# Performance work log

Hardware: AMD Instinct MI355X
Metric: run time of the kernel (lower is better)

The kernel has to match this reference:

```python
import jax, jax.numpy as jnp
import numpy as np

UP = 2
NUM_POINT = 9
GROUPS = 4


def pixel_shuffle(t, r):
    # [B, C*r*r, H, W] -> [B, C, H*r, W*r], torch layout: in[b, c*r*r + i*r + j, h, w] -> out[b, c, h*r+i, w*r+j]
    B, C, H, W = t.shape
    Co = C // (r * r)
    t = t.reshape(B, Co, r, r, H, W)
    t = t.transpose(0, 1, 4, 2, 5, 3)
    return t.reshape(B, Co, H * r, W * r)


def _bilinear_sample(feat, py, px):
    # feat: [E, H, W]; py, px: [P, Hup, Wup] in low-res pixel coords (zero padding outside)
    H, W = feat.shape[1], feat.shape[2]
    y0f = jnp.floor(py)
    x0f = jnp.floor(px)
    ty = py - y0f
    tx = px - x0f
    y0 = y0f.astype(jnp.int32)
    x0 = x0f.astype(jnp.int32)
    out = jnp.zeros(feat.shape[:1] + py.shape, dtype=feat.dtype)
    corners = ((0, 0, (1 - ty) * (1 - tx)), (0, 1, (1 - ty) * tx),
               (1, 0, ty * (1 - tx)), (1, 1, ty * tx))
    for dy, dx, w in corners:
        yi = y0 + dy
        xi = x0 + dx
        valid = ((yi >= 0) & (yi < H) & (xi >= 0) & (xi < W)).astype(feat.dtype)
        yc = jnp.clip(yi, 0, H - 1)
        xc = jnp.clip(xi, 0, W - 1)
        out = out + feat[:, yc, xc] * (w * valid)[None]
    return out  # [E, P, Hup, Wup]

# vmap over batch and group dims
_sample_bg = jax.vmap(jax.vmap(_bilinear_sample))


def setup_inputs() -> dict:
    key = jax.random.key(0)
    ks = jax.random.split(key, 8)
    B, Cy, Cx = 2, 256, 256
    H, W = 64, 64
    Hup, Wup = H * UP, W * UP
    GE = GROUPS * 32              # q/k channels = groups * embedding_dim
    OFF = GROUPS * NUM_POINT * 2 * UP * UP  # 288
    return {
        "y": jax.random.normal(ks[0], (B, Cy, Hup, Wup), jnp.float32),
        "x": jax.random.normal(ks[1], (B, Cx, H, W), jnp.float32),
        "Wq": jax.random.normal(ks[2], (GE, Cy), jnp.float32) * 0.02,
        "bq": jnp.zeros((GE,), jnp.float32),
        "Wk": jax.random.normal(ks[3], (GE, Cx), jnp.float32) * 0.02,
        "bk": jnp.zeros((GE,), jnp.float32),
        "Woff": jax.random.normal(ks[4], (OFF, Cx), jnp.float32) * 0.02,
        "boff": jnp.zeros((OFF,), jnp.float32),
    }


def reference(y, x, Wq, bq, Wk, bk, Woff, boff):
    G, P, up = GROUPS, NUM_POINT, UP
    B, C, H, W = x.shape
    # 1x1 convs as einsum
    q = jnp.einsum('oi,bihw->bohw', Wq, y) + bq[None, :, None, None]
    k = jnp.einsum('oi,bihw->bohw', Wk, x) + bk[None, :, None, None]
    off = jnp.einsum('oi,bihw->bohw', Woff, x) + boff[None, :, None, None]
    off = pixel_shuffle(off, up)  # [B, G*P*2, Hup, Wup]
    Hup, Wup = off.shape[2], off.shape[3]
    off = off.reshape(B, G, P, 2, Hup, Wup)
    # sampling positions in low-res coordinates: align-centers base + learned offset
    base_y = (jnp.arange(Hup, dtype=jnp.float32) + 0.5) / up - 0.5
    base_x = (jnp.arange(Wup, dtype=jnp.float32) + 0.5) / up - 0.5
    py = off[:, :, :, 0] + base_y[None, None, None, :, None]  # [B,G,P,Hup,Wup]
    px = off[:, :, :, 1] + base_x[None, None, None, None, :]
    E = Wq.shape[0] // G
    qg = q.reshape(B, G, E, Hup, Wup)
    kg = k.reshape(B, G, E, H, W)
    # deform_qk: gather k at offset points, dot with q over embedding dim
    ks = _sample_bg(kg, py, px)                    # [B,G,E,P,Hup,Wup]
    attn = jnp.einsum('bgehw,bgephw->bgphw', qg, ks)
    attn = jax.nn.softmax(attn, axis=2)            # softmax over points
    # deform_av: gather x at the same points, weighted sum by attn
    Cg = C // G
    xg = x.reshape(B, G, Cg, H, W)
    xs = _sample_bg(xg, py, px)                    # [B,G,Cg,P,Hup,Wup]
    out = jnp.einsum('bgphw,bgcphw->bgchw', attn, xs)
    return out.reshape(B, C, Hup, Wup)
```

## Files before the change

### kernel.cpp

```cpp
#include <hip/hip_runtime.h>

#define B_N   2
#define H_LR  64
#define W_LR  64
#define HUP   128
#define WUP   128
#define GRP   4
#define NPT   9
#define EMB   32
#define CGRP  64
#define KIN   256
#define GE    128
#define NOFF  288

typedef __attribute__((ext_vector_type(8))) short short8v;
typedef _Float16 half8v __attribute__((ext_vector_type(8)));
typedef __attribute__((ext_vector_type(4))) float f32x4;

__device__ __forceinline__ ushort f2bf(float f) {
    unsigned u = __float_as_uint(f);
    u += 0x7FFFu + ((u >> 16) & 1u);
    return (ushort)(u >> 16);
}
__device__ __forceinline__ float bf2f(ushort h) {
    return __uint_as_float(((unsigned)h) << 16);
}
__device__ __forceinline__ ushort f2h(float f) {
    _Float16 h = (_Float16)f;
    return __builtin_bit_cast(ushort, h);
}
__device__ __forceinline__ float h2f(ushort u) {
    _Float16 h = __builtin_bit_cast(_Float16, u);
    return (float)h;
}

__global__ __launch_bounds__(256) void convert_w_kernel(
    const float* __restrict__ Wq, const float* __restrict__ Wk,
    const float* __restrict__ Woff, ushort* __restrict__ wqbf,
    ushort* __restrict__ wkobf)
{
    int r = blockIdx.x, k = threadIdx.x;
    if (r < 128) {
        wqbf[r * 256 + k] = f2bf(Wq[r * 256 + k]);
    } else {
        int r2 = r - 128;
        float v = 0.f;
        if (r2 < 128) v = Wk[r2 * 256 + k];
        else if (r2 < 416) v = Woff[(r2 - 128) * 256 + k];
        wkobf[r2 * 256 + k] = f2bf(v);
    }
}

__global__ __launch_bounds__(256, 4) void mfma_gemm(
    const float* __restrict__ y, const float* __restrict__ x,
    const ushort* __restrict__ WQ, const ushort* __restrict__ WKO,
    const float* __restrict__ bq, const float* __restrict__ bk,
    const float* __restrict__ boff,
    ushort* __restrict__ qbf, ushort* __restrict__ kbf,
    float* __restrict__ offw)
{
    __shared__ __align__(16) ushort sY[64][68];
    __shared__ __align__(16) ushort sB[128][72];

    int bid = blockIdx.x;
    const float* SRC; const ushort* WBF; const float* ba; const float* bb;
    ushort* OBF; float* OFP;
    int M, m0, n0, b;
    if (bid < 512) {
        int mt = bid & 255; b = bid >> 8;
        SRC = y; WBF = WQ; ba = bq; bb = nullptr; OBF = qbf; OFP = nullptr;
        M = 16384; m0 = mt * 64; n0 = 0;
    } else {
        int r = bid - 512;
        int mt = r & 63, nt2 = (r >> 6) & 3; b = r >> 8;
        SRC = x; WBF = WKO; ba = bk; bb = boff; OBF = kbf; OFP = offw;
        M = 4096; m0 = mt * 64; n0 = nt2 * 128;
    }

    int tid = threadIdx.x;
    int lane = tid & 63;
    int wv = tid >> 6, wm = wv >> 1, wn = wv & 1;
    int il = lane & 15, g4 = lane >> 4;
    int st_m4 = tid & 15, st_c = tid >> 4;
    int st_c8 = tid & 7,  st_n = tid >> 3;

    f32x4 acc[2][4];
#pragma unroll
    for (int i = 0; i < 2; ++i)
#pragma unroll
        for (int j = 0; j < 4; ++j) { f32x4 z = {0.f,0.f,0.f,0.f}; acc[i][j] = z; }

    const float* src_b = SRC + (size_t)b * KIN * M;

    float4 ra[4]; short8v rb[4];
#pragma unroll
    for (int i = 0; i < 4; ++i)
        ra[i] = *(const float4*)&src_b[(size_t)(st_c + i * 16) * M + m0 + st_m4 * 4];
#pragma unroll
    for (int i = 0; i < 4; ++i)
        rb[i] = *(const short8v*)&WBF[(size_t)(n0 + st_n + i * 32) * KIN + st_c8 * 8];

    for (int ks = 0; ks < 4; ++ks) {
#pragma unroll
        for (int i = 0; i < 4; ++i) {
            ushort4 h;
            h.x = f2bf(ra[i].x); h.y = f2bf(ra[i].y);
            h.z = f2bf(ra[i].z); h.w = f2bf(ra[i].w);
            *(ushort4*)&sY[st_c + i * 16][st_m4 * 4] = h;
            *(short8v*)&sB[st_n + i * 32][st_c8 * 8] = rb[i];
        }
        __syncthreads();
        if (ks < 3) {
            int k0 = (ks + 1) * 64;
#pragma unroll
            for (int i = 0; i < 4; ++i)
                ra[i] = *(const float4*)&src_b[(size_t)(k0 + st_c + i * 16) * M + m0 + st_m4 * 4];
#pragma unroll
            for (int i = 0; i < 4; ++i)
                rb[i] = *(const short8v*)&WBF[(size_t)(n0 + st_n + i * 32) * KIN + k0 + st_c8 * 8];
        }
#pragma unroll
        for (int kc = 0; kc < 2; ++kc) {
            int kb = kc * 32 + g4 * 8;
            short8v af[2], bfr[4];
#pragma unroll
            for (int mf = 0; mf < 2; ++mf) {
                int m = wm * 32 + mf * 16 + il;
                short8v t;
#pragma unroll
                for (int j = 0; j < 8; ++j) t[j] = (short)sY[kb + j][m];
                af[mf] = t;
            }
#pragma unroll
            for (int nf = 0; nf < 4; ++nf)
                bfr[nf] = *(const short8v*)&sB[wn * 64 + nf * 16 + il][kb];
#pragma unroll
            for (int mf = 0; mf < 2; ++mf)
#pragma unroll
                for (int nf = 0; nf < 4; ++nf)
                    acc[mf][nf] = __builtin_amdgcn_mfma_f32_16x16x32_bf16(
                        af[mf], bfr[nf], acc[mf][nf], 0, 0, 0);
        }
        __syncthreads();
    }

#pragma unroll
    for (int mf = 0; mf < 2; ++mf) {
#pragma unroll
        for (int r = 0; r < 4; ++r) {
            int m = m0 + wm * 32 + mf * 16 + g4 * 4 + r;
            size_t row = (size_t)b * M + m;
#pragma unroll
            for (int nf = 0; nf < 4; ++nf) {
                int n = n0 + wn * 64 + nf * 16 + il;
                float v = acc[mf][nf][r];
                if (n < GE) {
                    OBF[row * 128 + n] = f2bf(v + ba[n]);
                } else {
                    int no = n - GE;
                    if (no < NOFF) OFP[row * 288 + no] = v + bb[no];
                }
            }
        }
    }
}

#define RROWS 6
#define RCOLS 11
#define RPX   66

__global__ __launch_bounds__(256, 4) void deform_kernel(
    const ushort* __restrict__ qbf,
    const ushort* __restrict__ kbf,
    const float* __restrict__ offw,
    const float* __restrict__ x,
    float* __restrict__ out)
{
    __shared__ __align__(16) ushort sXt[64][96];
    __shared__ __align__(16) ushort sK[66][40];
    __shared__ __align__(16) ushort sQ[64][40];
    __shared__ __align__(16) ushort sSW[64][72];
    __shared__ uint   sGt[576];
    __shared__ int    sGz[576];
    __shared__ float  sAttn[576];
    __shared__ int    sFB[129];

    int bx = blockIdx.x;
    int tw = bx & 7, th = (bx >> 3) & 31, g = (bx >> 8) & 3, b = bx >> 10;
    int tid = threadIdx.x;
    int wv_ = tid >> 6, lane = tid & 63;
    int row = lane & 15, kb8 = lane >> 4;

    const int ry0 = th * 2 - 2, rx0 = tw * 8 - 1;
    float* sOff = (float*)&sSW[0][0];

    if (tid == 0) sFB[0] = 0;
    for (int i = tid; i < 960; i += 256) {
        int r = i / 15, j = i - (i / 15) * 15;
        *(uint*)&sXt[r][66 + j * 2] = 0;
    }
    for (int s = tid; s < 384; s += 256) {
        int gy = s % 6, ch = s / 6;
        int gyg = min(max(ry0 + gy, 0), 63);
        const float* xr = x + ((size_t)b * 256 + g * CGRP + ch) * 4096 + gyg * 64;
        ushort* dst = &sXt[ch][gy * RCOLS];
        if (tw >= 1 && tw <= 6) {
            int a0 = rx0 - 3;
            float v[16];
#pragma unroll
            for (int t4 = 0; t4 < 4; ++t4) {
                float4 f = *(const float4*)&xr[a0 + t4 * 4];
                v[t4*4+0] = f.x; v[t4*4+1] = f.y; v[t4*4+2] = f.z; v[t4*4+3] = f.w;
            }
#pragma unroll
            for (int qx = 0; qx < RCOLS; ++qx) dst[qx] = f2h(v[qx + 3]);
        } else {
#pragma unroll
            for (int qx = 0; qx < RCOLS; ++qx) {
                int gxg = min(max(rx0 + qx, 0), 63);
                dst[qx] = f2h(xr[gxg]);
            }
        }
    }
    for (int i = tid; i < 264; i += 256) {
        int rp = i >> 2, c4 = i & 3;
        int qy = rp / RCOLS, qx = rp - qy * RCOLS;
        int gy = min(max(ry0 + qy, 0), 63), gx = min(max(rx0 + qx, 0), 63);
        *(short8v*)&sK[rp][c4 * 8] =
            *(const short8v*)&kbf[((size_t)b * 4096 + gy * 64 + gx) * 128 +
                                  g * EMB + c4 * 8];
    }
    {
        int px = tid >> 2, c4 = tid & 3;
        int hup = th * 4 + (px >> 4), wup = tw * 16 + (px & 15);
        *(short8v*)&sQ[px][c4 * 8] =
            *(const short8v*)&qbf[((size_t)b * 16384 + hup * 128 + wup) * 128 +
                                  g * EMB + c4 * 8];
    }
    for (int i = tid; i < 288; i += 256) {
        int lr = i / 18, f4 = i - (i / 18) * 18;
        int yy = th * 2 + (lr >> 3), xx = tw * 8 + (lr & 7);
        *(float4*)&sOff[lr * 72 + f4 * 4] =
            *(const float4*)&offw[((size_t)b * 4096 + yy * 64 + xx) * 288 +
                                  g * 72 + f4 * 4];
    }
    __syncthreads();

    f32x4 sreg[5];
    {
        short8v a = *(const short8v*)&sQ[wv_ * 16 + row][kb8 * 8];
#pragma unroll
        for (int nt = 0; nt < 5; ++nt) {
            int rr = nt * 16 + row; if (rr > 65) rr = 65;
            short8v bf = *(const short8v*)&sK[rr][kb8 * 8];
            f32x4 z = {0.f, 0.f, 0.f, 0.f};
            sreg[nt] = __builtin_amdgcn_mfma_f32_16x16x32_bf16(a, bf, z, 0, 0, 0);
        }
    }
    for (int item = tid; item < 576; item += 256) {
        int px = item / 9, pt = item - (item / 9) * 9;
        int lx = px & 15, ly = px >> 4;
        int hup = th * 4 + ly, wup = tw * 16 + lx;
        int lr = (ly >> 1) * 8 + (lx >> 1);
        int ij = ((hup & 1) << 1) | (wup & 1);
        float offy = sOff[lr * 72 + pt * 8 + ij];
        float offx = sOff[lr * 72 + pt * 8 + 4 + ij];
        float py  = offy + hup * 0.5f - 0.25f;
        float pxx = offx + wup * 0.5f - 0.25f;
        float y0f = floorf(py), x0f = floorf(pxx);
        float ty = py - y0f, tx = pxx - x0f;
        int y0 = (int)y0f, x0 = (int)x0f;
        int mk = 0;
        if ((unsigned)y0 < 64u && (unsigned)x0 < 64u)         mk |= 1;
        if ((unsigned)y0 < 64u && (unsigned)(x0+1) < 64u)     mk |= 2;
        if ((unsigned)(y0+1) < 64u && (unsigned)x0 < 64u)     mk |= 4;
        if ((unsigned)(y0+1) < 64u && (unsigned)(x0+1) < 64u) mk |= 8;
        int iy = y0 - ry0, ix = x0 - rx0;
        bool inreg = ((unsigned)iy <= (unsigned)(RROWS - 2)) &&
                     ((unsigned)ix <= (unsigned)(RCOLS - 2));
        int fl, zp;
        if (!mk)        { fl = 16; zp = 0; }
        else if (inreg) { fl = mk | 16; zp = iy * RCOLS + ix; }
        else            { fl = mk; zp = (y0 + 1) * 66 + (x0 + 1); }
        sGt[item] = (uint)f2h(ty) | ((uint)f2h(tx) << 16);
        sGz[item] = (zp << 5) | fl;
    }
    __syncthreads();

#pragma unroll
    for (int nt = 0; nt < 5; ++nt) {
        int rp = nt * 16 + row;
        if (rp < RPX) {
#pragma unroll
            for (int r = 0; r < 4; ++r)
                sSW[wv_ * 16 + kb8 * 4 + r][rp] = f2h(sreg[nt][r]);
        }
    }
    __syncthreads();

    for (int item = tid; item < 576; item += 256) {
        int px = item / 9;
        uint gt = sGt[item];
        float ty = h2f((ushort)gt), tx = h2f((ushort)(gt >> 16));
        int z = sGz[item];
        int fl = z & 31;
        float a;
        if (fl & 16) {
            int zi = z >> 5;
            float w00 = (1.f - ty) * (1.f - tx), w01 = (1.f - ty) * tx;
            float w10 = ty * (1.f - tx), w11 = ty * tx;
            a  = (fl & 1) ? w00 * h2f(sSW[px][zi])             : 0.f;
            a += (fl & 2) ? w01 * h2f(sSW[px][zi + 1])         : 0.f;
            a += (fl & 4) ? w10 * h2f(sSW[px][zi + RCOLS])     : 0.f;
            a += (fl & 8) ? w11 * h2f(sSW[px][zi + RCOLS + 1]) : 0.f;
        } else {
            int t = z >> 5;
            int y0 = t / 66 - 1, x0 = t - (t / 66) * 66 - 1;
            a = 0.f;
#pragma unroll
            for (int c = 0; c < 4; ++c) if ((fl >> c) & 1) {
                int dy = c >> 1, dx = c & 1;
                float wgt = (dy ? ty : 1.f - ty) * (dx ? tx : 1.f - tx);
                const ushort* kr = &kbf[((size_t)b * 4096 + (y0 + dy) * 64 + x0 + dx) * 128 +
                                        g * EMB];
                float dot = 0.f;
                for (int e = 0; e < EMB; ++e) dot += bf2f(sQ[px][e]) * bf2f(kr[e]);
                a += wgt * dot;
            }
            int old = atomicAdd(&sFB[0], 1);
            if (old < 128) sFB[1 + old] = item;
        }
        sAttn[item] = a;
    }
    __syncthreads();

    if (tid < 64) {
        float aa[NPT];
        float mx = -1e30f;
#pragma unroll
        for (int p = 0; p < NPT; ++p) { aa[p] = sAttn[tid * 9 + p]; mx = fmaxf(mx, aa[p]); }
        float s = 0.f;
#pragma unroll
        for (int p = 0; p < NPT; ++p) { aa[p] = __expf(aa[p] - mx); s += aa[p]; }
        float inv = 1.f / s;
#pragma unroll
        for (int p = 0; p < NPT; ++p) sAttn[tid * 9 + p] = aa[p] * inv;
    } else {
        float4* p = (float4*)&sSW[0][0];
        float4 z4 = make_float4(0.f, 0.f, 0.f, 0.f);
        for (int i = tid - 64; i < 576; i += 192) p[i] = z4;
    }
    __syncthreads();

    if (tid < 64) {
        int px = tid;
#pragma unroll
        for (int pt = 0; pt < NPT; ++pt) {
            int item = px * 9 + pt;
            int z = sGz[item];
            int fl = z & 31;
            if (!(fl & 16)) continue;
            uint gt = sGt[item];
            float ty = h2f((ushort)gt), tx = h2f((ushort)(gt >> 16));
            float a = sAttn[item];
            int zi = z >> 5;
            ushort* c = &sSW[px][zi];
            if (fl & 1) c[0]         = f2h(h2f(c[0])         + (1.f-ty)*(1.f-tx)*a);
            if (fl & 2) c[1]         = f2h(h2f(c[1])         + (1.f-ty)*tx*a);
            if (fl & 4) c[RCOLS]     = f2h(h2f(c[RCOLS])     + ty*(1.f-tx)*a);
            if (fl & 8) c[RCOLS + 1] = f2h(h2f(c[RCOLS + 1]) + ty*tx*a);
        }
    }
    __syncthreads();

    {
        half8v bfm[3][4];
#pragma unroll
        for (int kt = 0; kt < 3; ++kt)
#pragma unroll
            for (int nt = 0; nt < 4; ++nt)
                bfm[kt][nt] = *(const half8v*)&sXt[nt * 16 + row][kt * 32 + kb8 * 8];

        int px = wv_ * 16 + row;
        half8v af0 = *(const half8v*)&sSW[px][kb8 * 8];
        half8v af1 = *(const half8v*)&sSW[px][32 + kb8 * 8];
        half8v af2 = {0,0,0,0,0,0,0,0};
        if (kb8 == 0) af2 = *(const half8v*)&sSW[px][64];

        f32x4 acc[4];
#pragma unroll
        for (int nt = 0; nt < 4; ++nt) { f32x4 z = {0.f,0.f,0.f,0.f}; acc[nt] = z; }
#pragma unroll
        for (int nt = 0; nt < 4; ++nt) {
            acc[nt] = __builtin_amdgcn_mfma_f32_16x16x32_f16(af0, bfm[0][nt], acc[nt], 0, 0, 0);
            acc[nt] = __builtin_amdgcn_mfma_f32_16x16x32_f16(af1, bfm[1][nt], acc[nt], 0, 0, 0);
            acc[nt] = __builtin_amdgcn_mfma_f32_16x16x32_f16(af2, bfm[2][nt], acc[nt], 0, 0, 0);
        }
        int hup = th * 4 + wv_;
#pragma unroll
        for (int nt = 0; nt < 4; ++nt) {
            int ch = nt * 16 + row;
            float* ob = out + ((size_t)b * 256 + g * CGRP + ch) * 16384 +
                        hup * 128 + tw * 16 + kb8 * 4;
#pragma unroll
            for (int r = 0; r < 4; ++r) ob[r] = acc[nt][r];
        }
    }
    __syncthreads();

    int nfb = min(sFB[0], 128);
    for (int i = 0; i < nfb; ++i) {
        if (tid < 64) {
            int item = sFB[1 + i];
            int px = item / 9;
            uint gt = sGt[item];
            float ty = h2f((ushort)gt), tx = h2f((ushort)(gt >> 16));
            int z = sGz[item];
            float a = sAttn[item];
            int fl = z & 15;
            int t = z >> 5;
            int y0 = t / 66 - 1, x0 = t - (t / 66) * 66 - 1;
            const float* xg = x + ((size_t)b * 256 + g * CGRP + tid) * 4096;
            float v = 0.f;
            if (fl & 1) v += (1.f-ty)*(1.f-tx)*a * xg[y0*64 + x0];
            if (fl & 2) v += (1.f-ty)*tx*a       * xg[y0*64 + x0 + 1];
            if (fl & 4) v += ty*(1.f-tx)*a       * xg[(y0+1)*64 + x0];
            if (fl & 8) v += ty*tx*a             * xg[(y0+1)*64 + x0 + 1];
            int hup = th * 4 + (px >> 4), wup = tw * 16 + (px & 15);
            float* op = out + ((size_t)b * 256 + g * CGRP + tid) * 16384 +
                        hup * 128 + wup;
            *op += v;
        }
    }
}

extern "C" void kernel_launch(void* const* d_in, const int* in_sizes, int n_in,
                              void* d_out, int out_size, void* d_ws, size_t ws_size,
                              hipStream_t stream)
{
    const float* y    = (const float*)d_in[0];
    const float* x    = (const float*)d_in[1];
    const float* Wq   = (const float*)d_in[2];
    const float* bq   = (const float*)d_in[3];
    const float* Wk   = (const float*)d_in[4];
    const float* bk   = (const float*)d_in[5];
    const float* Woff = (const float*)d_in[6];
    const float* boff = (const float*)d_in[7];
    float* out = (float*)d_out;

    ushort* wqbf  = (ushort*)d_ws;
    ushort* wkobf = wqbf + 128 * 256;
    ushort* qbf   = wkobf + 512 * 256;
    ushort* kbf   = qbf + (size_t)B_N * 16384 * 128;
    float*  offw  = (float*)(kbf + (size_t)B_N * 4096 * 128);

    convert_w_kernel<<<dim3(640), dim3(256), 0, stream>>>(Wq, Wk, Woff, wqbf, wkobf);

    mfma_gemm<<<dim3(1024), dim3(256), 0, stream>>>(
        y, x, wqbf, wkobf, bq, bk, boff, qbf, kbf, offw);

    deform_kernel<<<dim3(2048), dim3(256), 0, stream>>>(qbf, kbf, offw, x, out);
}
```

Before: 64.86 us.

## Fuse weight bf16 conversion into GEMM and trim deform MFMA tail

Drops the separate weight-conversion kernel. The GEMM now reads fp32 weights directly and converts them to bf16 while staging, which saves one launch and a workspace round trip but repeats the conversion in every block. In the deform kernel, the sXt row is narrowed and its zero-padding pass removed, and the x tile is written with packed 32-bit stores. The third MFMA over a mostly-zero K chunk is replaced by a two-term scalar FMA tail on the leftover columns.

```diff
diff --git a/kernel.cpp b/kernel.cpp
--- a/kernel.cpp
+++ b/kernel.cpp
@@ -34,26 +34,10 @@
     return (float)h;
 }
 
-__global__ __launch_bounds__(256) void convert_w_kernel(
-    const float* __restrict__ Wq, const float* __restrict__ Wk,
-    const float* __restrict__ Woff, ushort* __restrict__ wqbf,
-    ushort* __restrict__ wkobf)
-{
-    int r = blockIdx.x, k = threadIdx.x;
-    if (r < 128) {
-        wqbf[r * 256 + k] = f2bf(Wq[r * 256 + k]);
-    } else {
-        int r2 = r - 128;
-        float v = 0.f;
-        if (r2 < 128) v = Wk[r2 * 256 + k];
-        else if (r2 < 416) v = Woff[(r2 - 128) * 256 + k];
-        wkobf[r2 * 256 + k] = f2bf(v);
-    }
-}
-
 __global__ __launch_bounds__(256, 4) void mfma_gemm(
     const float* __restrict__ y, const float* __restrict__ x,
-    const ushort* __restrict__ WQ, const ushort* __restrict__ WKO,
+    const float* __restrict__ Wq, const float* __restrict__ Wk,
+    const float* __restrict__ Woff,
     const float* __restrict__ bq, const float* __restrict__ bk,
     const float* __restrict__ boff,
     ushort* __restrict__ qbf, ushort* __restrict__ kbf,
@@ -63,17 +47,18 @@
     __shared__ __align__(16) ushort sB[128][72];
 
     int bid = blockIdx.x;
-    const float* SRC; const ushort* WBF; const float* ba; const float* bb;
+    const float* SRC; const float* ba; const float* bb;
     ushort* OBF; float* OFP;
     int M, m0, n0, b;
-    if (bid < 512) {
+    bool isQ = (bid < 512);
+    if (isQ) {
         int mt = bid & 255; b = bid >> 8;
-        SRC = y; WBF = WQ; ba = bq; bb = nullptr; OBF = qbf; OFP = nullptr;
+        SRC = y; ba = bq; bb = nullptr; OBF = qbf; OFP = nullptr;
         M = 16384; m0 = mt * 64; n0 = 0;
     } else {
         int r = bid - 512;
         int mt = r & 63, nt2 = (r >> 6) & 3; b = r >> 8;
-        SRC = x; WBF = WKO; ba = bk; bb = boff; OBF = kbf; OFP = offw;
+        SRC = x; ba = bk; bb = boff; OBF = kbf; OFP = offw;
         M = 4096; m0 = mt * 64; n0 = nt2 * 128;
     }
 
@@ -84,6 +69,16 @@
     int st_m4 = tid & 15, st_c = tid >> 4;
     int st_c8 = tid & 7,  st_n = tid >> 3;
 
+    const float* wrowp[4];
+#pragma unroll
+    for (int i = 0; i < 4; ++i) {
+        int n = n0 + st_n + i * 32;
+        if (isQ)            wrowp[i] = Wq  + (size_t)n * KIN;
+        else if (n < GE)    wrowp[i] = Wk  + (size_t)n * KIN;
+        else if (n < GE + NOFF) wrowp[i] = Woff + (size_t)(n - GE) * KIN;
+        else                wrowp[i] = nullptr;
+    }
+
     f32x4 acc[2][4];
 #pragma unroll
     for (int i = 0; i < 2; ++i)
@@ -97,8 +92,16 @@
     for (int i = 0; i < 4; ++i)
         ra[i] = *(const float4*)&src_b[(size_t)(st_c + i * 16) * M + m0 + st_m4 * 4];
 #pragma unroll
-    for (int i = 0; i < 4; ++i)
-        rb[i] = *(const short8v*)&WBF[(size_t)(n0 + st_n + i * 32) * KIN + st_c8 * 8];
+    for (int i = 0; i < 4; ++i) {
+        short8v t = {0,0,0,0,0,0,0,0};
+        if (wrowp[i]) {
+            float4 a = *(const float4*)&wrowp[i][st_c8 * 8];
+            float4 c = *(const float4*)&wrowp[i][st_c8 * 8 + 4];
+            t[0]=(short)f2bf(a.x); t[1]=(short)f2bf(a.y); t[2]=(short)f2bf(a.z); t[3]=(short)f2bf(a.w);
+            t[4]=(short)f2bf(c.x); t[5]=(short)f2bf(c.y); t[6]=(short)f2bf(c.z); t[7]=(short)f2bf(c.w);
+        }
+        rb[i] = t;
+    }
 
     for (int ks = 0; ks < 4; ++ks) {
 #pragma unroll
@@ -116,8 +119,16 @@
             for (int i = 0; i < 4; ++i)
                 ra[i] = *(const float4*)&src_b[(size_t)(k0 + st_c + i * 16) * M + m0 + st_m4 * 4];
 #pragma unroll
-            for (int i = 0; i < 4; ++i)
-                rb[i] = *(const short8v*)&WBF[(size_t)(n0 + st_n + i * 32) * KIN + k0 + st_c8 * 8];
+            for (int i = 0; i < 4; ++i) {
+                short8v t = {0,0,0,0,0,0,0,0};
+                if (wrowp[i]) {
+                    float4 a = *(const float4*)&wrowp[i][k0 + st_c8 * 8];
+                    float4 c = *(const float4*)&wrowp[i][k0 + st_c8 * 8 + 4];
+                    t[0]=(short)f2bf(a.x); t[1]=(short)f2bf(a.y); t[2]=(short)f2bf(a.z); t[3]=(short)f2bf(a.w);
+                    t[4]=(short)f2bf(c.x); t[5]=(short)f2bf(c.y); t[6]=(short)f2bf(c.z); t[7]=(short)f2bf(c.w);
+                }
+                rb[i] = t;
+            }
         }
 #pragma unroll
         for (int kc = 0; kc < 2; ++kc) {
@@ -176,7 +187,7 @@
     const float* __restrict__ x,
     float* __restrict__ out)
 {
-    __shared__ __align__(16) ushort sXt[64][96];
+    __shared__ __align__(16) ushort sXt[64][72];
     __shared__ __align__(16) ushort sK[66][40];
     __shared__ __align__(16) ushort sQ[64][40];
     __shared__ __align__(16) ushort sSW[64][72];
@@ -195,31 +206,42 @@
     float* sOff = (float*)&sSW[0][0];
 
     if (tid == 0) sFB[0] = 0;
-    for (int i = tid; i < 960; i += 256) {
-        int r = i / 15, j = i - (i / 15) * 15;
-        *(uint*)&sXt[r][66 + j * 2] = 0;
-    }
     for (int s = tid; s < 384; s += 256) {
         int gy = s % 6, ch = s / 6;
         int gyg = min(max(ry0 + gy, 0), 63);
         const float* xr = x + ((size_t)b * 256 + g * CGRP + ch) * 4096 + gyg * 64;
-        ushort* dst = &sXt[ch][gy * RCOLS];
+        float v[11];
         if (tw >= 1 && tw <= 6) {
             int a0 = rx0 - 3;
-            float v[16];
+            float tmp[16];
 #pragma unroll
             for (int t4 = 0; t4 < 4; ++t4) {
                 float4 f = *(const float4*)&xr[a0 + t4 * 4];
-                v[t4*4+0] = f.x; v[t4*4+1] = f.y; v[t4*4+2] = f.z; v[t4*4+3] = f.w;
-            }
-#pragma unroll
-            for (int qx = 0; qx < RCOLS; ++qx) dst[qx] = f2h(v[qx + 3]);
+                tmp[t4*4+0] = f.x; tmp[t4*4+1] = f.y; tmp[t4*4+2] = f.z; tmp[t4*4+3] = f.w;
+            }
+#pragma unroll
+            for (int qx = 0; qx < RCOLS; ++qx) v[qx] = tmp[qx + 3];
         } else {
 #pragma unroll
             for (int qx = 0; qx < RCOLS; ++qx) {
                 int gxg = min(max(rx0 + qx, 0), 63);
-                dst[qx] = f2h(xr[gxg]);
-            }
+                v[qx] = xr[gxg];
+            }
+        }
+        ushort* dst = &sXt[ch][0];
+        int c0 = gy * RCOLS;
+        if (c0 & 1) {
+            dst[c0] = f2h(v[0]);
+#pragma unroll
+            for (int j = 0; j < 5; ++j)
+                *(uint*)&dst[c0 + 1 + 2*j] =
+                    (uint)f2h(v[1 + 2*j]) | ((uint)f2h(v[2 + 2*j]) << 16);
+        } else {
+#pragma unroll
+            for (int j = 0; j < 5; ++j)
+                *(uint*)&dst[c0 + 2*j] =
+                    (uint)f2h(v[2*j]) | ((uint)f2h(v[1 + 2*j]) << 16);
+            dst[c0 + 10] = f2h(v[10]);
         }
     }
     for (int i = tid; i < 264; i += 256) {
@@ -374,9 +396,9 @@
     __syncthreads();
 
     {
-        half8v bfm[3][4];
-#pragma unroll
-        for (int kt = 0; kt < 3; ++kt)
+        half8v bfm[2][4];
+#pragma unroll
+        for (int kt = 0; kt < 2; ++kt)
 #pragma unroll
             for (int nt = 0; nt < 4; ++nt)
                 bfm[kt][nt] = *(const half8v*)&sXt[nt * 16 + row][kt * 32 + kb8 * 8];
@@ -384,8 +406,6 @@
         int px = wv_ * 16 + row;
         half8v af0 = *(const half8v*)&sSW[px][kb8 * 8];
         half8v af1 = *(const half8v*)&sSW[px][32 + kb8 * 8];
-        half8v af2 = {0,0,0,0,0,0,0,0};
-        if (kb8 == 0) af2 = *(const half8v*)&sSW[px][64];
 
         f32x4 acc[4];
 #pragma unroll
@@ -394,7 +414,20 @@
         for (int nt = 0; nt < 4; ++nt) {
             acc[nt] = __builtin_amdgcn_mfma_f32_16x16x32_f16(af0, bfm[0][nt], acc[nt], 0, 0, 0);
             acc[nt] = __builtin_amdgcn_mfma_f32_16x16x32_f16(af1, bfm[1][nt], acc[nt], 0, 0, 0);
-            acc[nt] = __builtin_amdgcn_mfma_f32_16x16x32_f16(af2, bfm[2][nt], acc[nt], 0, 0, 0);
+        }
+        float wc[4][2];
+#pragma unroll
+        for (int r = 0; r < 4; ++r) {
+            uint u = *(uint*)&sSW[wv_ * 16 + kb8 * 4 + r][64];
+            wc[r][0] = h2f((ushort)u); wc[r][1] = h2f((ushort)(u >> 16));
+        }
+#pragma unroll
+        for (int nt = 0; nt < 4; ++nt) {
+            uint u = *(uint*)&sXt[nt * 16 + row][64];
+            float x0 = h2f((ushort)u), x1 = h2f((ushort)(u >> 16));
+#pragma unroll
+            for (int r = 0; r < 4; ++r)
+                acc[nt][r] += wc[r][0] * x0 + wc[r][1] * x1;
         }
         int hup = th * 4 + wv_;
 #pragma unroll
@@ -448,16 +481,12 @@
     const float* boff = (const float*)d_in[7];
     float* out = (float*)d_out;
 
-    ushort* wqbf  = (ushort*)d_ws;
-    ushort* wkobf = wqbf + 128 * 256;
-    ushort* qbf   = wkobf + 512 * 256;
+    ushort* qbf   = (ushort*)d_ws;
     ushort* kbf   = qbf + (size_t)B_N * 16384 * 128;
     float*  offw  = (float*)(kbf + (size_t)B_N * 4096 * 128);
 
-    convert_w_kernel<<<dim3(640), dim3(256), 0, stream>>>(Wq, Wk, Woff, wqbf, wkobf);
-
     mfma_gemm<<<dim3(1024), dim3(256), 0, stream>>>(
-        y, x, wqbf, wkobf, bq, bk, boff, qbf, kbf, offw);
+        y, x, Wq, Wk, Woff, bq, bk, boff, qbf, kbf, offw);
 
     deform_kernel<<<dim3(2048), dim3(256), 0, stream>>>(qbf, kbf, offw, x, out);
 }
```

New measurement: 63.99 us. Within noise of the previous version (-1.3%).
